# Performance work log

Measured on AMD Instinct MI355X. Metric: run time of the kernel, lower is better.

## Reference

```python
import jax, jax.numpy as jnp
import numpy as np

DIM = 256
HEADS = 4


def setup_inputs() -> dict:
    key = jax.random.key(0)
    k1, k2, k3, k4, k5 = jax.random.split(key, 5)
    x = jax.random.normal(k1, (8, DIM, 128, 128), dtype=jnp.float32)
    s_in = 1.0 / np.sqrt(DIM)
    Wqkv = jax.random.normal(k2, (DIM, 3 * DIM), dtype=jnp.float32) * s_in
    bqkv = jax.random.normal(k3, (3 * DIM,), dtype=jnp.float32) * 0.02
    Wproj = jax.random.normal(k4, (DIM, DIM), dtype=jnp.float32) * s_in
    bproj = jax.random.normal(k5, (DIM,), dtype=jnp.float32) * 0.02
    return {"x": x, "Wqkv": Wqkv, "bqkv": bqkv, "Wproj": Wproj, "bproj": bproj}


def reference(x, Wqkv, bqkv, Wproj, bproj):
    b, c, h, w = x.shape
    hd = c // HEADS  # head dim
    scale = hd ** -0.5
    # axis='h': (b c h w) -> (b*w, h, c)
    x_r = jnp.transpose(x, (0, 3, 2, 1)).reshape(b * w, h, c)
    qkv = x_r @ Wqkv + bqkv                              # [B, S, 3c]
    qkv = qkv.reshape(b * w, h, 3, HEADS, hd)
    qkv = jnp.transpose(qkv, (2, 0, 3, 1, 4))            # [3, B, H, S, d]
    q, k, v = qkv[0], qkv[1], qkv[2]
    attn = jax.nn.softmax(jnp.einsum('bhqd,bhkd->bhqk', q, k) * scale, axis=-1)
    out = jnp.einsum('bhqk,bhkd->bhqd', attn, v)         # [B, H, S, d]
    out = jnp.transpose(out, (0, 2, 1, 3)).reshape(b * w, h, c)
    out = out @ Wproj + bproj
    # (b*w, h, c) -> (b, c, h, w)
    out = out.reshape(b, w, h, c)
    return jnp.transpose(out, (0, 3, 2, 1))
```

## Files before the change

kernel.cpp:

```cpp
#include <hip/hip_runtime.h>


typedef _Float16 h4 __attribute__((ext_vector_type(4)));
typedef _Float16 h8 __attribute__((ext_vector_type(8)));
typedef float f4 __attribute__((ext_vector_type(4)));
typedef unsigned int u4 __attribute__((ext_vector_type(4)));

#define MFMA32(a, b, c) __builtin_amdgcn_mfma_f32_16x16x32_f16((a), (b), (c), 0, 0, 0)

__device__ __forceinline__ void gll16(const _Float16* g, _Float16* l) {
  __builtin_amdgcn_global_load_lds(
      (const __attribute__((address_space(1))) void*)g,
      (__attribute__((address_space(3))) void*)l, 16, 0, 0);
}

__global__ __launch_bounds__(256) void prep_w(const float* __restrict__ Wqkv,
                                              const float* __restrict__ Wproj,
                                              _Float16* __restrict__ wqt,
                                              _Float16* __restrict__ wpt) {
  int i = blockIdx.x * 256 + threadIdx.x;
  if (i < 768 * 256) {
    int f = i >> 8, c = i & 255;
    wqt[i] = (_Float16)Wqkv[c * 768 + f];
  } else {
    int j = i - 768 * 256;
    int f = j >> 8, c = j & 255;
    wpt[j] = (_Float16)Wproj[c * 256 + f];
  }
}

__global__ __launch_bounds__(256, 4) void k1f(const float* __restrict__ x,
                                              const _Float16* __restrict__ wqt,
                                              const float* __restrict__ bqkv,
                                              _Float16* __restrict__ qkv,
                                              int b_base, int nb) {
  const int wg = blockIdx.x;
  const int xcd = wg & 7, seq = wg >> 3;
  const int id = xcd * (nb * 32) + seq;
  const int hb = id & 127;
  const int rest = id >> 7;
  const int wh = rest & 1, bl = rest >> 1;
  const int b = b_base + bl;
  const int w0 = wh * 64;

  const int tid = threadIdx.x;
  const int lane = tid & 63, wv = tid >> 6;
  const int g = lane >> 4, l16 = lane & 15;
  const int wr = wv >> 1, wc = wv & 1;

  __shared__ __align__(16) char smem[34816];
  _Float16* sXT = (_Float16*)smem;
  _Float16* sA = (_Float16*)smem;
  _Float16* sO = (_Float16*)(smem + 16384);

  {
    const int j0 = tid & 7, r8 = tid >> 3;
#pragma unroll
    for (int p = 0; p < 8; ++p) {
      const int c = p * 32 + r8;
      const float* src = x + (((long)b * 256 + c) * 128 + hb) * 128 + w0;
      f4 v0 = *(const f4*)(src + j0 * 4);
      f4 v1 = *(const f4*)(src + (j0 + 8) * 4);
#pragma unroll
      for (int i = 0; i < 4; ++i) {
        sXT[(j0 * 4 + i) * 264 + c] = (_Float16)v0[i];
        sXT[((j0 + 8) * 4 + i) * 264 + c] = (_Float16)v1[i];
      }
    }
  }
  __syncthreads();

  h8 bfr[4][2][2];
#pragma unroll
  for (int kc = 0; kc < 4; ++kc)
#pragma unroll
    for (int ks = 0; ks < 2; ++ks)
#pragma unroll
      for (int nt = 0; nt < 2; ++nt) {
        const int t = wc * 32 + nt * 16 + l16;
        bfr[kc][ks][nt] =
            *(const h8*)(sXT + t * 264 + kc * 64 + ks * 32 + 8 * g);
      }
  __syncthreads();

  const int r0 = wv * 32;
  const int rl = lane >> 3, ch = (lane & 7) * 8;
  const int wl = tid >> 2, dc = tid & 3;

  for (int ft = 0; ft < 6; ++ft) {
    const int f0 = ft * 128;
    f4 acc[4][2];
#pragma unroll
    for (int mt = 0; mt < 4; ++mt)
#pragma unroll
      for (int nt = 0; nt < 2; ++nt)
#pragma unroll
        for (int r = 0; r < 4; ++r) acc[mt][nt][r] = 0.f;

    for (int kc = 0; kc < 4; ++kc) {
#pragma unroll
      for (int i = 0; i < 4; ++i) {
        const int row = r0 + i * 8 + rl;
        gll16(wqt + (long)(f0 + row) * 256 + kc * 64 + ch, sA + (r0 + i * 8) * 64);
      }
      __syncthreads();
#pragma unroll
      for (int ks = 0; ks < 2; ++ks) {
        h8 af[4];
#pragma unroll
        for (int mt = 0; mt < 4; ++mt)
          af[mt] = *(const h8*)(sA + (wr * 64 + mt * 16 + l16) * 64 + ks * 32 + 8 * g);
#pragma unroll
        for (int mt = 0; mt < 4; ++mt)
#pragma unroll
          for (int nt = 0; nt < 2; ++nt)
            acc[mt][nt] = MFMA32(af[mt], bfr[kc][ks][nt], acc[mt][nt]);
      }
      __syncthreads();
    }

#pragma unroll
    for (int mt = 0; mt < 4; ++mt) {
      f4 bb = *(const f4*)(bqkv + f0 + wr * 64 + mt * 16 + 4 * g);
#pragma unroll
      for (int nt = 0; nt < 2; ++nt) {
        const int tl = wc * 32 + nt * 16 + l16;
#pragma unroll
        for (int r = 0; r < 4; ++r)
          sO[tl * 136 + wr * 64 + mt * 16 + 4 * g + r] =
              (_Float16)(acc[mt][nt][r] + bb[r]);
      }
    }
    __syncthreads();
#pragma unroll
    for (int h2 = 0; h2 < 2; ++h2) {
      const int fh = f0 + h2 * 64;
      const int qi = fh >> 8, head = (fh >> 6) & 3;
      _Float16* dst = qkv + (((long)(qi * nb + bl) * 4 + head) * 128 + w0 + wl) * 8192 +
                      hb * 64 + dc * 16;
      const _Float16* s = sO + wl * 136 + h2 * 64 + dc * 16;
      *(u4*)dst = *(const u4*)s;
      *(u4*)(dst + 8) = *(const u4*)(s + 8);
    }
    __syncthreads();
  }
}

__global__ __launch_bounds__(256) void k2_attn(const _Float16* __restrict__ qkv,
                                               _Float16* __restrict__ attnout,
                                               int nb) {
  const int w = blockIdx.x, head = blockIdx.y, bl = blockIdx.z;
  const int tid = threadIdx.x;
  const int lane = tid & 63, wv = tid >> 6;
  const int g = lane >> 4, l16 = lane & 15;

  __shared__ __align__(16) char smem[(128 * 72 * 2 + 64 * 136) * 2];
  _Float16* sQ = (_Float16*)smem;
  _Float16* sK = sQ + 128 * 72;
  _Float16* sVT = sK + 128 * 72;
  _Float16* sP = sQ;
  _Float16* sO = sQ;

  const long base = (((long)bl * 4 + head) * 128 + w) * 8192;
  const long QS = (long)nb * 4 * 128 * 8192;
  const _Float16* qg = qkv + base;
  const _Float16* kg = qkv + base + QS;
  const _Float16* vg = qkv + base + 2 * QS;

#pragma unroll
  for (int i = 0; i < 4; ++i) {
    int u = tid + 256 * i;
    int hh = u >> 3, dq = u & 7;
    *(u4*)(sQ + hh * 72 + dq * 8) = *(const u4*)(qg + hh * 64 + dq * 8);
    *(u4*)(sK + hh * 72 + dq * 8) = *(const u4*)(kg + hh * 64 + dq * 8);
  }
  {
    const int hh = tid & 127, dcv = tid >> 7;
#pragma unroll
    for (int jj = 0; jj < 4; ++jj) {
      u4 vv = *(const u4*)(vg + hh * 64 + dcv * 32 + jj * 8);
      const _Float16* pe = (const _Float16*)&vv;
#pragma unroll
      for (int e = 0; e < 8; ++e)
        sVT[(dcv * 32 + jj * 8 + e) * 136 + hh] = pe[e];
    }
  }
  __syncthreads();

  f4 accS[8][2];
  for (int i = 0; i < 8; ++i)
    for (int jt = 0; jt < 2; ++jt)
      for (int r = 0; r < 4; ++r) accS[i][jt][r] = 0.f;
#pragma unroll
  for (int ks = 0; ks < 2; ++ks) {
    const int k = ks * 32 + 8 * g;
    h8 af[8], bf[2];
#pragma unroll
    for (int i = 0; i < 8; ++i)
      af[i] = *(const h8*)(sK + (i * 16 + l16) * 72 + k);
#pragma unroll
    for (int jt = 0; jt < 2; ++jt)
      bf[jt] = *(const h8*)(sQ + (wv * 32 + jt * 16 + l16) * 72 + k);
#pragma unroll
    for (int i = 0; i < 8; ++i)
#pragma unroll
      for (int jt = 0; jt < 2; ++jt)
        accS[i][jt] = MFMA32(af[i], bf[jt], accS[i][jt]);
  }

  float rinv[2];
#pragma unroll
  for (int jt = 0; jt < 2; ++jt) {
    float m = -1e30f;
    for (int i = 0; i < 8; ++i)
      for (int r = 0; r < 4; ++r) m = fmaxf(m, accS[i][jt][r]);
    m = fmaxf(m, __shfl_xor(m, 16));
    m = fmaxf(m, __shfl_xor(m, 32));
    float s = 0.f;
    for (int i = 0; i < 8; ++i)
      for (int r = 0; r < 4; ++r) {
        float p = __expf((accS[i][jt][r] - m) * 0.125f);
        accS[i][jt][r] = p;
        s += p;
      }
    s += __shfl_xor(s, 16);
    s += __shfl_xor(s, 32);
    rinv[jt] = 1.0f / s;
  }

  __syncthreads();
#pragma unroll
  for (int jt = 0; jt < 2; ++jt) {
    const int hq = wv * 32 + jt * 16 + l16;
#pragma unroll
    for (int i = 0; i < 8; ++i) {
      h4 pv;
      pv[0] = (_Float16)accS[i][jt][0];
      pv[1] = (_Float16)accS[i][jt][1];
      pv[2] = (_Float16)accS[i][jt][2];
      pv[3] = (_Float16)accS[i][jt][3];
      *(h4*)(sP + hq * 136 + i * 16 + 4 * g) = pv;
    }
  }
  __syncthreads();

  f4 accO[4][2];
  for (int mt = 0; mt < 4; ++mt)
    for (int jt = 0; jt < 2; ++jt)
      for (int r = 0; r < 4; ++r) accO[mt][jt][r] = 0.f;
#pragma unroll
  for (int i2 = 0; i2 < 4; ++i2) {
    const int k = i2 * 32 + 8 * g;
    h8 av[4], pb[2];
#pragma unroll
    for (int mt = 0; mt < 4; ++mt)
      av[mt] = *(const h8*)(sVT + (mt * 16 + l16) * 136 + k);
#pragma unroll
    for (int jt = 0; jt < 2; ++jt)
      pb[jt] = *(const h8*)(sP + (wv * 32 + jt * 16 + l16) * 136 + k);
#pragma unroll
    for (int mt = 0; mt < 4; ++mt)
#pragma unroll
      for (int jt = 0; jt < 2; ++jt)
        accO[mt][jt] = MFMA32(av[mt], pb[jt], accO[mt][jt]);
  }

  __syncthreads();
#pragma unroll
  for (int mt = 0; mt < 4; ++mt)
#pragma unroll
    for (int jt = 0; jt < 2; ++jt)
#pragma unroll
      for (int r = 0; r < 4; ++r)
        sO[(wv * 32 + jt * 16 + l16) * 72 + mt * 16 + 4 * g + r] =
            (_Float16)(accO[mt][jt][r] * rinv[jt]);
  __syncthreads();

  const int hh = tid >> 1, d0 = (tid & 1) * 32;
  const _Float16* s = sO + hh * 72 + d0;
  _Float16* dst = attnout + ((long)bl * 16384 + hh * 128 + w) * 256 + head * 64 + d0;
#pragma unroll
  for (int e = 0; e < 4; ++e)
    *(u4*)(dst + e * 8) = *(const u4*)(s + e * 8);
}

__global__ __launch_bounds__(256, 4) void k3_proj(const _Float16* __restrict__ attnout,
                                                  const _Float16* __restrict__ wpt,
                                                  const float* __restrict__ bproj,
                                                  float* __restrict__ out,
                                                  int b_base, int nb) {
  const int ct = blockIdx.x, tt = blockIdx.y, bl = blockIdx.z;
  const int b = b_base + bl;
  const int tid = threadIdx.x;
  const int lane = tid & 63, wv = tid >> 6;
  const int g = lane >> 4, l16 = lane & 15;
  const int wr = wv >> 1, wc = wv & 1;
  const int co0 = ct * 128;
  const long t0 = (long)tt * 128;

  __shared__ __align__(16) char smem[33792];
  _Float16* sA = (_Float16*)smem;
  _Float16* sB = sA + 128 * 64;
  float* sOut = (float*)smem;

  f4 acc[4][4];
#pragma unroll
  for (int mt = 0; mt < 4; ++mt)
#pragma unroll
    for (int nt = 0; nt < 4; ++nt)
#pragma unroll
      for (int r = 0; r < 4; ++r) acc[mt][nt][r] = 0.f;

  const _Float16* Ab = wpt + (long)co0 * 256;
  const _Float16* Bb = attnout + ((long)bl * 16384 + t0) * 256;
  const int r0 = wv * 32;
  const int rl = lane >> 3, ch = (lane & 7) * 8;

  for (int kc = 0; kc < 4; ++kc) {
    const int c0 = kc * 64;
#pragma unroll
    for (int i = 0; i < 4; ++i) {
      const int row = r0 + i * 8 + rl;
      gll16(Ab + (long)row * 256 + c0 + ch, sA + (r0 + i * 8) * 64);
      gll16(Bb + (long)row * 256 + c0 + ch, sB + (r0 + i * 8) * 64);
    }
    __syncthreads();
#pragma unroll
    for (int ks = 0; ks < 2; ++ks) {
      const int k = ks * 32 + 8 * g;
      h8 af[4], bf[4];
#pragma unroll
      for (int mt = 0; mt < 4; ++mt)
        af[mt] = *(const h8*)(sA + (wr * 64 + mt * 16 + l16) * 64 + k);
#pragma unroll
      for (int nt = 0; nt < 4; ++nt)
        bf[nt] = *(const h8*)(sB + (wc * 64 + nt * 16 + l16) * 64 + k);
#pragma unroll
      for (int mt = 0; mt < 4; ++mt)
#pragma unroll
        for (int nt = 0; nt < 4; ++nt)
          acc[mt][nt] = MFMA32(af[mt], bf[nt], acc[mt][nt]);
    }
    __syncthreads();
  }

#pragma unroll
  for (int h2 = 0; h2 < 2; ++h2) {
    if (h2) __syncthreads();
    if (wr == h2) {
#pragma unroll
      for (int mt = 0; mt < 4; ++mt) {
        f4 bb = *(const f4*)(bproj + co0 + h2 * 64 + mt * 16 + 4 * g);
#pragma unroll
        for (int nt = 0; nt < 4; ++nt)
#pragma unroll
          for (int r = 0; r < 4; ++r)
            sOut[(mt * 16 + 4 * g + r) * 132 + wc * 64 + nt * 16 + l16] =
                acc[mt][nt][r] + bb[r];
      }
    }
    __syncthreads();
    const int row = tid >> 2, seg = (tid & 3) * 32;
    const float* s = sOut + row * 132 + seg;
    float* dst = out + ((long)b * 256 + co0 + h2 * 64 + row) * 16384 + t0 + seg;
#pragma unroll
    for (int e = 0; e < 8; ++e)
      *(f4*)(dst + e * 4) = *(const f4*)(s + e * 4);
  }
}

extern "C" void kernel_launch(void* const* d_in, const int* in_sizes, int n_in,
                              void* d_out, int out_size, void* d_ws, size_t ws_size,
                              hipStream_t stream) {
  const float* x = (const float*)d_in[0];
  const float* Wqkv = (const float*)d_in[1];
  const float* bqkv = (const float*)d_in[2];
  const float* Wproj = (const float*)d_in[3];
  const float* bproj = (const float*)d_in[4];
  float* out = (float*)d_out;

  char* ws = (char*)d_ws;
  const long WQT = 393216L, WPT = 131072L;
  const long PER_B = 25165824L + 8388608L;
  long nb_l = ((long)ws_size - (WQT + WPT)) / PER_B;
  int nb = nb_l < 1 ? 1 : (nb_l > 8 ? 8 : (int)nb_l);

  _Float16* wqt = (_Float16*)ws;
  _Float16* wpt = (_Float16*)(ws + WQT);
  _Float16* qkv = (_Float16*)(ws + WQT + WPT);
  _Float16* attnout = (_Float16*)(ws + WQT + WPT + (long)nb * 25165824L);

  prep_w<<<1024, 256, 0, stream>>>(Wqkv, Wproj, wqt, wpt);

  for (int b0 = 0; b0 < 8; b0 += nb) {
    int nbv = (8 - b0 < nb) ? (8 - b0) : nb;
    k1f<<<nbv * 256, 256, 0, stream>>>(x, wqt, bqkv, qkv, b0, nbv);
    k2_attn<<<dim3(128, 4, nbv), 256, 0, stream>>>(qkv, attnout, nbv);
    k3_proj<<<dim3(2, 128, nbv), 256, 0, stream>>>(attnout, wpt, bproj, out, b0, nbv);
  }
}
```

Before: 249.5 us.

## Pre-swizzle QKV weights into MFMA fragment order and load directly from global

The QKV weight preprocessing now writes the transposed fp16 weights in per-lane MFMA A-fragment order. The QKV projection kernel loads its A fragments straight from global memory (L2-resident) instead of staging them through LDS with global_load_lds and two barriers per k-chunk. This removes LDS traffic and synchronisation from the inner loop and shrinks shared memory. The price is more global/L2 loads per wave, since the two column-waves each fetch the same fragments, and more live registers; occupancy is lowered to 3 waves-groups per CU via launch bounds.

Result: slower. 271.9 us (+8.9%).

```diff
diff --git a/kernel.cpp b/kernel.cpp
--- a/kernel.cpp
+++ b/kernel.cpp
@@ -16,21 +16,24 @@
 
 __global__ __launch_bounds__(256) void prep_w(const float* __restrict__ Wqkv,
                                               const float* __restrict__ Wproj,
-                                              _Float16* __restrict__ wqt,
+                                              _Float16* __restrict__ wqtf,
                                               _Float16* __restrict__ wpt) {
   int i = blockIdx.x * 256 + threadIdx.x;
   if (i < 768 * 256) {
     int f = i >> 8, c = i & 255;
-    wqt[i] = (_Float16)Wqkv[c * 768 + f];
+    int ft = f >> 7, wr = (f >> 6) & 1, mt = (f >> 4) & 3, l16 = f & 15;
+    int kc = c >> 6, ks = (c >> 5) & 1, gg = (c >> 3) & 3, j = c & 7;
+    int frag = (ft * 2 + wr) * 32 + mt * 8 + kc * 2 + ks;
+    wqtf[(long)frag * 512 + (gg * 16 + l16) * 8 + j] = (_Float16)Wqkv[c * 768 + f];
   } else {
-    int j = i - 768 * 256;
-    int f = j >> 8, c = j & 255;
-    wpt[j] = (_Float16)Wproj[c * 256 + f];
-  }
-}
-
-__global__ __launch_bounds__(256, 4) void k1f(const float* __restrict__ x,
-                                              const _Float16* __restrict__ wqt,
+    int jj = i - 768 * 256;
+    int f = jj >> 8, c = jj & 255;
+    wpt[jj] = (_Float16)Wproj[c * 256 + f];
+  }
+}
+
+__global__ __launch_bounds__(256, 3) void k1f(const float* __restrict__ x,
+                                              const _Float16* __restrict__ wqtf,
                                               const float* __restrict__ bqkv,
                                               _Float16* __restrict__ qkv,
                                               int b_base, int nb) {
@@ -48,10 +51,9 @@
   const int g = lane >> 4, l16 = lane & 15;
   const int wr = wv >> 1, wc = wv & 1;
 
-  __shared__ __align__(16) char smem[34816];
+  __shared__ __align__(16) char smem[33792];
   _Float16* sXT = (_Float16*)smem;
-  _Float16* sA = (_Float16*)smem;
-  _Float16* sO = (_Float16*)(smem + 16384);
+  _Float16* sO = (_Float16*)smem;
 
   {
     const int j0 = tid & 7, r8 = tid >> 3;
@@ -83,8 +85,6 @@
       }
   __syncthreads();
 
-  const int r0 = wv * 32;
-  const int rl = lane >> 3, ch = (lane & 7) * 8;
   const int wl = tid >> 2, dc = tid & 3;
 
   for (int ft = 0; ft < 6; ++ft) {
@@ -97,27 +97,21 @@
 #pragma unroll
         for (int r = 0; r < 4; ++r) acc[mt][nt][r] = 0.f;
 
-    for (int kc = 0; kc < 4; ++kc) {
-#pragma unroll
-      for (int i = 0; i < 4; ++i) {
-        const int row = r0 + i * 8 + rl;
-        gll16(wqt + (long)(f0 + row) * 256 + kc * 64 + ch, sA + (r0 + i * 8) * 64);
-      }
-      __syncthreads();
+    const _Float16* Af = wqtf + (long)(ft * 2 + wr) * 32 * 512 + lane * 8;
+#pragma unroll
+    for (int kc = 0; kc < 4; ++kc)
 #pragma unroll
       for (int ks = 0; ks < 2; ++ks) {
         h8 af[4];
 #pragma unroll
         for (int mt = 0; mt < 4; ++mt)
-          af[mt] = *(const h8*)(sA + (wr * 64 + mt * 16 + l16) * 64 + ks * 32 + 8 * g);
+          af[mt] = *(const h8*)(Af + (mt * 8 + kc * 2 + ks) * 512);
 #pragma unroll
         for (int mt = 0; mt < 4; ++mt)
 #pragma unroll
           for (int nt = 0; nt < 2; ++nt)
             acc[mt][nt] = MFMA32(af[mt], bfr[kc][ks][nt], acc[mt][nt]);
       }
-      __syncthreads();
-    }
 
 #pragma unroll
     for (int mt = 0; mt < 4; ++mt) {
@@ -385,16 +379,16 @@
   long nb_l = ((long)ws_size - (WQT + WPT)) / PER_B;
   int nb = nb_l < 1 ? 1 : (nb_l > 8 ? 8 : (int)nb_l);
 
-  _Float16* wqt = (_Float16*)ws;
+  _Float16* wqtf = (_Float16*)ws;
   _Float16* wpt = (_Float16*)(ws + WQT);
   _Float16* qkv = (_Float16*)(ws + WQT + WPT);
   _Float16* attnout = (_Float16*)(ws + WQT + WPT + (long)nb * 25165824L);
 
-  prep_w<<<1024, 256, 0, stream>>>(Wqkv, Wproj, wqt, wpt);
+  prep_w<<<1024, 256, 0, stream>>>(Wqkv, Wproj, wqtf, wpt);
 
   for (int b0 = 0; b0 < 8; b0 += nb) {
     int nbv = (8 - b0 < nb) ? (8 - b0) : nb;
-    k1f<<<nbv * 256, 256, 0, stream>>>(x, wqt, bqkv, qkv, b0, nbv);
+    k1f<<<nbv * 256, 256, 0, stream>>>(x, wqtf, bqkv, qkv, b0, nbv);
     k2_attn<<<dim3(128, 4, nbv), 256, 0, stream>>>(qkv, attnout, nbv);
     k3_proj<<<dim3(2, 128, nbv), 256, 0, stream>>>(attnout, wpt, bproj, out, b0, nbv);
   }
```
